# Performance work log

Hardware: AMD Instinct MI355X
Metric: run time of the kernel (lower is better)

Reference implementation:

```python
import jax, jax.numpy as jnp
import numpy as np

N = 256  # node_num, fully-connected graph
NEG_SLOPE = 0.2


def _edges(n):
    # fully-connected permutations; PyG GATConv removes then re-adds self-loops,
    # so effectively all n*n (src, dst) pairs are present.
    idx = jnp.arange(n)
    src = jnp.repeat(idx, n)
    dst = jnp.tile(idx, n)
    return src, dst


def _gat_conv(x, W, att_src, att_dst, b, src, dst, n):
    # x: [N, Fin], W: [Fin, H*C], att_*: [H, C], b: [H*C]
    H, C = att_src.shape
    h = (x @ W).reshape(n, H, C)                       # [N, H, C]
    a_src = jnp.einsum('nhc,hc->nh', h, att_src)       # [N, H]
    a_dst = jnp.einsum('nhc,hc->nh', h, att_dst)
    e = jax.nn.leaky_relu(a_src[src] + a_dst[dst], NEG_SLOPE)  # [E, H]
    # segment softmax over incoming edges of each dst node
    m = jax.ops.segment_max(e, dst, num_segments=n)    # [N, H]
    p = jnp.exp(e - m[dst])
    denom = jax.ops.segment_sum(p, dst, num_segments=n)
    alpha = p / (denom[dst] + 1e-16)                   # [E, H]
    msg = h[src] * alpha[:, :, None]                   # [E, H, C]
    out = jax.ops.segment_sum(msg, dst, num_segments=n)  # [N, H, C]
    return out.reshape(n, H * C) + b


def setup_inputs() -> dict:
    key = jax.random.key(0)
    ks = jax.random.split(key, 7)
    Fin, H1, C1 = 128, 4, 128
    s = lambda fan: 1.0 / np.sqrt(fan)
    return {
        'x': jax.random.normal(ks[0], (8, N, Fin), dtype=jnp.float32),
        'W1': jax.random.normal(ks[1], (Fin, H1 * C1), dtype=jnp.float32) * s(Fin),
        'att_src1': jax.random.normal(ks[2], (H1, C1), dtype=jnp.float32) * s(C1),
        'att_dst1': jax.random.normal(ks[3], (H1, C1), dtype=jnp.float32) * s(C1),
        'b1': jnp.zeros((H1 * C1,), dtype=jnp.float32),
        'W2': jax.random.normal(ks[4], (H1 * C1, Fin), dtype=jnp.float32) * s(H1 * C1),
        'att_src2': jax.random.normal(ks[5], (1, Fin), dtype=jnp.float32) * s(Fin),
        'att_dst2': jax.random.normal(ks[6], (1, Fin), dtype=jnp.float32) * s(Fin),
        'b2': jnp.zeros((Fin,), dtype=jnp.float32),
    }


def reference(x, W1, att_src1, att_dst1, b1, W2, att_src2, att_dst2, b2):
    src, dst = _edges(N)

    def one_graph(xi):
        h = jax.nn.relu(_gat_conv(xi, W1, att_src1, att_dst1, b1, src, dst, N))
        return _gat_conv(h, W2, att_src2, att_dst2, b2, src, dst, N)

    return jax.vmap(one_graph)(x)  # [B, N, Fin]
```

## Files before the change

kernel.cpp:

```cpp
#include <hip/hip_runtime.h>
#include <hip/hip_bf16.h>

#define BATCH 8
#define NN    256
#define FIN   128
#define H1    4
#define C1    128
#define HC1   512
#define NEG_SLOPE 0.2f

__global__ void gemm1_kernel(const float* __restrict__ x,
                             const float* __restrict__ W1,
                             float* __restrict__ h1) {
    __shared__ float xs[8][FIN];
    const int b  = blockIdx.y;
    const int r0 = blockIdx.x * 8;
    const int t  = threadIdx.x;

    const float* xp = x + (b * NN + r0) * FIN;
    #pragma unroll
    for (int i = 0; i < 4; ++i) {
        int idx = t + i * 256;
        xs[idx >> 7][idx & 127] = xp[idx];
    }
    __syncthreads();

    float acc[8][2];
    #pragma unroll
    for (int r = 0; r < 8; ++r) { acc[r][0] = 0.f; acc[r][1] = 0.f; }

    for (int k = 0; k < FIN; ++k) {
        float w0 = W1[k * HC1 + t];
        float w1 = W1[k * HC1 + t + 256];
        #pragma unroll
        for (int r = 0; r < 8; ++r) {
            float xv = xs[r][k];
            acc[r][0] = fmaf(xv, w0, acc[r][0]);
            acc[r][1] = fmaf(xv, w1, acc[r][1]);
        }
    }
    #pragma unroll
    for (int r = 0; r < 8; ++r) {
        h1[(b * NN + r0 + r) * HC1 + t]       = acc[r][0];
        h1[(b * NN + r0 + r) * HC1 + t + 256] = acc[r][1];
    }
}

__global__ void areduce1_kernel(const float* __restrict__ h1,
                                const float* __restrict__ att_src,
                                const float* __restrict__ att_dst,
                                float* __restrict__ a_src,
                                float* __restrict__ a_dst) {
    const int bn   = blockIdx.x;
    const int t    = threadIdx.x;
    const int h    = t >> 6;
    const int lane = t & 63;

    const float* hp = h1 + bn * HC1 + h * C1;
    float v0 = hp[lane], v1 = hp[lane + 64];
    float s = v0 * att_src[h * C1 + lane] + v1 * att_src[h * C1 + lane + 64];
    float d = v0 * att_dst[h * C1 + lane] + v1 * att_dst[h * C1 + lane + 64];
    #pragma unroll
    for (int off = 32; off > 0; off >>= 1) {
        s += __shfl_down(s, off, 64);
        d += __shfl_down(d, off, 64);
    }
    if (lane == 0) {
        a_src[bn * H1 + h] = s;
        a_dst[bn * H1 + h] = d;
    }
}

__global__ void agg1_kernel(const float* __restrict__ h1,
                            const float* __restrict__ a_src,
                            const float* __restrict__ a_dst,
                            const float* __restrict__ b1,
                            float* __restrict__ hrelu) {
    __shared__ float s_as[NN];
    __shared__ float s_ad[16];
    __shared__ float sp[16][NN];
    __shared__ float red[16][17];
    __shared__ float s_m[16], s_den[16];

    const int b    = blockIdx.z;
    const int head = blockIdx.y;
    const int d0   = blockIdx.x * 16;
    const int t    = threadIdx.x;

    s_as[t] = a_src[(b * NN + t) * H1 + head];
    if (t < 16) s_ad[t] = a_dst[(b * NN + d0 + t) * H1 + head];
    __syncthreads();

    const int d = t >> 4;
    const int l = t & 15;
    const float adst = s_ad[d];

    float mx = -1e30f;
    #pragma unroll
    for (int i = 0; i < 16; ++i) {
        int src = l + i * 16;
        float e = s_as[src] + adst;
        e = (e > 0.f) ? e : NEG_SLOPE * e;
        sp[d][src] = e;
        mx = fmaxf(mx, e);
    }
    red[d][l] = mx;
    __syncthreads();
    if (t < 16) {
        float m = red[t][0];
        #pragma unroll
        for (int i = 1; i < 16; ++i) m = fmaxf(m, red[t][i]);
        s_m[t] = m;
    }
    __syncthreads();

    const float m = s_m[d];
    float sum = 0.f;
    #pragma unroll
    for (int i = 0; i < 16; ++i) {
        int src = l + i * 16;
        float p = __expf(sp[d][src] - m);
        sp[d][src] = p;
        sum += p;
    }
    red[d][l] = sum;
    __syncthreads();
    if (t < 16) {
        float s = 0.f;
        #pragma unroll
        for (int i = 0; i < 16; ++i) s += red[t][i];
        s_den[t] = s + 1e-16f;
    }
    __syncthreads();

    const int c = t & 127;
    const int g = t >> 7;
    float acc[8];
    #pragma unroll
    for (int j = 0; j < 8; ++j) acc[j] = 0.f;

    const float* hbase = h1 + (size_t)(b * NN) * HC1 + head * C1 + c;
    for (int src = 0; src < NN; ++src) {
        float hv = hbase[(size_t)src * HC1];
        #pragma unroll
        for (int j = 0; j < 8; ++j)
            acc[j] = fmaf(sp[g * 8 + j][src], hv, acc[j]);
    }

    const float bias = b1[head * C1 + c];
    #pragma unroll
    for (int j = 0; j < 8; ++j) {
        int dst = d0 + g * 8 + j;
        float v = acc[j] / s_den[g * 8 + j] + bias;
        hrelu[(b * NN + dst) * HC1 + head * C1 + c] = fmaxf(v, 0.f);
    }
}

__global__ void gemm2_kernel(const float* __restrict__ hrelu,
                             const float* __restrict__ W2,
                             float* __restrict__ h2) {
    __shared__ float xs[8][HC1];
    const int b  = blockIdx.y;
    const int r0 = blockIdx.x * 8;
    const int t  = threadIdx.x;

    const float* xp = hrelu + (size_t)(b * NN + r0) * HC1;
    #pragma unroll
    for (int i = 0; i < 16; ++i) {
        int idx = t + i * 256;
        xs[idx >> 9][idx & 511] = xp[idx];
    }
    __syncthreads();

    const int c  = t & 127;
    const int rg = t >> 7;
    float acc[4];
    #pragma unroll
    for (int i = 0; i < 4; ++i) acc[i] = 0.f;

    for (int k = 0; k < HC1; ++k) {
        float w = W2[k * FIN + c];
        #pragma unroll
        for (int i = 0; i < 4; ++i)
            acc[i] = fmaf(xs[rg * 4 + i][k], w, acc[i]);
    }
    #pragma unroll
    for (int i = 0; i < 4; ++i)
        h2[(b * NN + r0 + rg * 4 + i) * FIN + c] = acc[i];
}

__global__ void areduce2_kernel(const float* __restrict__ h2,
                                const float* __restrict__ att_src,
                                const float* __restrict__ att_dst,
                                float* __restrict__ a_src,
                                float* __restrict__ a_dst) {
    const int t    = threadIdx.x;
    const int bn   = blockIdx.x * 4 + (t >> 6);
    const int lane = t & 63;

    const float* hp = h2 + bn * FIN;
    float v0 = hp[lane], v1 = hp[lane + 64];
    float s = v0 * att_src[lane] + v1 * att_src[lane + 64];
    float d = v0 * att_dst[lane] + v1 * att_dst[lane + 64];
    #pragma unroll
    for (int off = 32; off > 0; off >>= 1) {
        s += __shfl_down(s, off, 64);
        d += __shfl_down(d, off, 64);
    }
    if (lane == 0) {
        a_src[bn] = s;
        a_dst[bn] = d;
    }
}

__global__ void agg2_kernel(const float* __restrict__ h2,
                            const float* __restrict__ a_src,
                            const float* __restrict__ a_dst,
                            const float* __restrict__ b2,
                            float* __restrict__ out) {
    __shared__ float s_as[NN];
    __shared__ float s_ad[8];
    __shared__ float sp[8][NN];
    __shared__ float red[8][33];
    __shared__ float s_m[8], s_den[8];

    const int b  = blockIdx.y;
    const int d0 = blockIdx.x * 8;
    const int t  = threadIdx.x;

    s_as[t] = a_src[b * NN + t];
    if (t < 8) s_ad[t] = a_dst[b * NN + d0 + t];
    __syncthreads();

    const int d = t >> 5;
    const int l = t & 31;
    const float adst = s_ad[d];

    float mx = -1e30f;
    #pragma unroll
    for (int i = 0; i < 8; ++i) {
        int src = l + i * 32;
        float e = s_as[src] + adst;
        e = (e > 0.f) ? e : NEG_SLOPE * e;
        sp[d][src] = e;
        mx = fmaxf(mx, e);
    }
    red[d][l] = mx;
    __syncthreads();
    if (t < 8) {
        float m = red[t][0];
        #pragma unroll
        for (int i = 1; i < 32; ++i) m = fmaxf(m, red[t][i]);
        s_m[t] = m;
    }
    __syncthreads();

    const float m = s_m[d];
    float sum = 0.f;
    #pragma unroll
    for (int i = 0; i < 8; ++i) {
        int src = l + i * 32;
        float p = __expf(sp[d][src] - m);
        sp[d][src] = p;
        sum += p;
    }
    red[d][l] = sum;
    __syncthreads();
    if (t < 8) {
        float s = 0.f;
        #pragma unroll
        for (int i = 0; i < 32; ++i) s += red[t][i];
        s_den[t] = s + 1e-16f;
    }
    __syncthreads();

    const int c = t & 127;
    const int g = t >> 7;
    float acc[4];
    #pragma unroll
    for (int j = 0; j < 4; ++j) acc[j] = 0.f;

    const float* hbase = h2 + (size_t)(b * NN) * FIN + c;
    for (int src = 0; src < NN; ++src) {
        float hv = hbase[(size_t)src * FIN];
        #pragma unroll
        for (int j = 0; j < 4; ++j)
            acc[j] = fmaf(sp[g * 4 + j][src], hv, acc[j]);
    }

    const float bias = b2[c];
    #pragma unroll
    for (int j = 0; j < 4; ++j) {
        int dst = d0 + g * 4 + j;
        out[(b * NN + dst) * FIN + c] = acc[j] / s_den[g * 4 + j] + bias;
    }
}

extern "C" void kernel_launch(void* const* d_in, const int* in_sizes, int n_in,
                              void* d_out, int out_size, void* d_ws, size_t ws_size,
                              hipStream_t stream) {
    const float* x    = (const float*)d_in[0];
    const float* W1   = (const float*)d_in[1];
    const float* as1  = (const float*)d_in[2];
    const float* ad1  = (const float*)d_in[3];
    const float* b1   = (const float*)d_in[4];
    const float* W2   = (const float*)d_in[5];
    const float* as2  = (const float*)d_in[6];
    const float* ad2  = (const float*)d_in[7];
    const float* b2   = (const float*)d_in[8];
    float* out = (float*)d_out;

    float* ws = (float*)d_ws;
    float* h1     = ws;
    float* hrelu  = ws + 1048576;
    float* h2     = ws + 2097152;
    float* a_src1 = ws + 2359296;
    float* a_dst1 = ws + 2367488;
    float* a_src2 = ws + 2375680;
    float* a_dst2 = ws + 2377728;

    gemm1_kernel<<<dim3(32, BATCH), 256, 0, stream>>>(x, W1, h1);
    areduce1_kernel<<<BATCH * NN, 256, 0, stream>>>(h1, as1, ad1, a_src1, a_dst1);
    agg1_kernel<<<dim3(16, H1, BATCH), 256, 0, stream>>>(h1, a_src1, a_dst1, b1, hrelu);
    gemm2_kernel<<<dim3(32, BATCH), 256, 0, stream>>>(hrelu, W2, h2);
    areduce2_kernel<<<BATCH * NN / 4, 256, 0, stream>>>(h2, as2, ad2, a_src2, a_dst2);
    agg2_kernel<<<dim3(32, BATCH), 256, 0, stream>>>(h2, a_src2, a_dst2, b2, out);
}
```

Before: 141.4 us.

## Fuse attention-score reductions into GEMMs and retile aggregation kernels

Folds the per-node attention dot products (a_src/a_dst) into the epilogues of both GEMM kernels, which removes two separate launches and the re-read of h1/h2. All kernels move to 512-thread blocks with fewer rows per block, giving more blocks and more parallelism. The softmax reductions now use wave shuffles instead of shared-memory serial reductions, which cuts barriers. The trade-off is less register reuse per thread: each W or h load now feeds fewer accumulators, so memory traffic per FMA goes up.

```diff
diff --git a/kernel.cpp b/kernel.cpp
--- a/kernel.cpp
+++ b/kernel.cpp
@@ -9,305 +9,212 @@
 #define HC1   512
 #define NEG_SLOPE 0.2f
 
-__global__ void gemm1_kernel(const float* __restrict__ x,
-                             const float* __restrict__ W1,
-                             float* __restrict__ h1) {
-    __shared__ float xs[8][FIN];
-    const int b  = blockIdx.y;
-    const int r0 = blockIdx.x * 8;
-    const int t  = threadIdx.x;
-
-    const float* xp = x + (b * NN + r0) * FIN;
-    #pragma unroll
-    for (int i = 0; i < 4; ++i) {
-        int idx = t + i * 256;
-        xs[idx >> 7][idx & 127] = xp[idx];
-    }
-    __syncthreads();
-
-    float acc[8][2];
-    #pragma unroll
-    for (int r = 0; r < 8; ++r) { acc[r][0] = 0.f; acc[r][1] = 0.f; }
-
+__device__ __forceinline__ float lrelu(float v) {
+    return v > 0.f ? v : NEG_SLOPE * v;
+}
+
+__global__ __launch_bounds__(512, 4)
+void gemm1_fused(const float* __restrict__ x, const float* __restrict__ W1,
+                 const float* __restrict__ as1, const float* __restrict__ ad1,
+                 float* __restrict__ h1, float* __restrict__ a_src,
+                 float* __restrict__ a_dst) {
+    __shared__ float xs[4][FIN];
+    __shared__ float redS[4][8], redD[4][8];
+    const int b = blockIdx.y, r0 = blockIdx.x * 4, t = threadIdx.x;
+
+    xs[t >> 7][t & 127] = x[(b * NN + r0) * FIN + t];
+    __syncthreads();
+
+    float a0 = 0.f, a1 = 0.f, a2 = 0.f, a3 = 0.f;
+    #pragma unroll 8
     for (int k = 0; k < FIN; ++k) {
-        float w0 = W1[k * HC1 + t];
-        float w1 = W1[k * HC1 + t + 256];
+        float w = W1[k * HC1 + t];
+        a0 = fmaf(xs[0][k], w, a0);
+        a1 = fmaf(xs[1][k], w, a1);
+        a2 = fmaf(xs[2][k], w, a2);
+        a3 = fmaf(xs[3][k], w, a3);
+    }
+    float acc[4] = {a0, a1, a2, a3};
+    #pragma unroll
+    for (int r = 0; r < 4; ++r)
+        h1[(b * NN + r0 + r) * HC1 + t] = acc[r];
+
+    const float as = as1[t], ad = ad1[t];
+    const int w = t >> 6, lane = t & 63;
+    #pragma unroll
+    for (int r = 0; r < 4; ++r) {
+        float s = acc[r] * as, d = acc[r] * ad;
         #pragma unroll
-        for (int r = 0; r < 8; ++r) {
-            float xv = xs[r][k];
-            acc[r][0] = fmaf(xv, w0, acc[r][0]);
-            acc[r][1] = fmaf(xv, w1, acc[r][1]);
+        for (int off = 32; off > 0; off >>= 1) {
+            s += __shfl_down(s, off, 64);
+            d += __shfl_down(d, off, 64);
         }
-    }
-    #pragma unroll
-    for (int r = 0; r < 8; ++r) {
-        h1[(b * NN + r0 + r) * HC1 + t]       = acc[r][0];
-        h1[(b * NN + r0 + r) * HC1 + t + 256] = acc[r][1];
-    }
-}
-
-__global__ void areduce1_kernel(const float* __restrict__ h1,
-                                const float* __restrict__ att_src,
-                                const float* __restrict__ att_dst,
-                                float* __restrict__ a_src,
-                                float* __restrict__ a_dst) {
-    const int bn   = blockIdx.x;
-    const int t    = threadIdx.x;
-    const int h    = t >> 6;
-    const int lane = t & 63;
-
-    const float* hp = h1 + bn * HC1 + h * C1;
-    float v0 = hp[lane], v1 = hp[lane + 64];
-    float s = v0 * att_src[h * C1 + lane] + v1 * att_src[h * C1 + lane + 64];
-    float d = v0 * att_dst[h * C1 + lane] + v1 * att_dst[h * C1 + lane + 64];
+        if (lane == 0) { redS[r][w] = s; redD[r][w] = d; }
+    }
+    __syncthreads();
+    if (t < 16) {
+        int r = t & 3, h = t >> 2;
+        a_src[(b * NN + r0 + r) * H1 + h] = redS[r][2 * h] + redS[r][2 * h + 1];
+        a_dst[(b * NN + r0 + r) * H1 + h] = redD[r][2 * h] + redD[r][2 * h + 1];
+    }
+}
+
+__global__ __launch_bounds__(512, 4)
+void agg1_kernel(const float* __restrict__ h1, const float* __restrict__ a_src,
+                 const float* __restrict__ a_dst, const float* __restrict__ b1,
+                 float* __restrict__ hrelu) {
+    __shared__ float s_as[NN];
+    __shared__ float s_ad[16];
+    __shared__ float sp[16][NN];
+    __shared__ float s_den[16];
+
+    const int b = blockIdx.z, head = blockIdx.y, d0 = blockIdx.x * 16;
+    const int t = threadIdx.x;
+
+    if (t < NN) s_as[t] = a_src[(b * NN + t) * H1 + head];
+    if (t < 16) s_ad[t] = a_dst[(b * NN + d0 + t) * H1 + head];
+    __syncthreads();
+
+    const int d = t >> 5, l = t & 31;
+    const float adst = s_ad[d];
+    float e[8];
+    float mx = -1e30f;
+    #pragma unroll
+    for (int i = 0; i < 8; ++i) {
+        float v = lrelu(s_as[l + i * 32] + adst);
+        e[i] = v;
+        mx = fmaxf(mx, v);
+    }
+    #pragma unroll
+    for (int off = 16; off > 0; off >>= 1)
+        mx = fmaxf(mx, __shfl_down(mx, off, 32));
+    mx = __shfl(mx, 0, 32);
+    float sum = 0.f;
+    #pragma unroll
+    for (int i = 0; i < 8; ++i) {
+        float p = __expf(e[i] - mx);
+        sp[d][l + i * 32] = p;
+        sum += p;
+    }
+    #pragma unroll
+    for (int off = 16; off > 0; off >>= 1)
+        sum += __shfl_down(sum, off, 32);
+    if (l == 0) s_den[d] = sum + 1e-16f;
+    __syncthreads();
+
+    const int c = t & 127, g = t >> 7;
+    float c0 = 0.f, c1 = 0.f, c2 = 0.f, c3 = 0.f;
+    const float* hb = h1 + (size_t)(b * NN) * HC1 + head * C1 + c;
+    #pragma unroll 4
+    for (int src = 0; src < NN; ++src) {
+        float hv = hb[(size_t)src * HC1];
+        c0 = fmaf(sp[g * 4 + 0][src], hv, c0);
+        c1 = fmaf(sp[g * 4 + 1][src], hv, c1);
+        c2 = fmaf(sp[g * 4 + 2][src], hv, c2);
+        c3 = fmaf(sp[g * 4 + 3][src], hv, c3);
+    }
+    float accs[4] = {c0, c1, c2, c3};
+    const float bias = b1[head * C1 + c];
+    #pragma unroll
+    for (int j = 0; j < 4; ++j) {
+        int dst = d0 + g * 4 + j;
+        float v = accs[j] / s_den[g * 4 + j] + bias;
+        hrelu[(b * NN + dst) * HC1 + head * C1 + c] = fmaxf(v, 0.f);
+    }
+}
+
+__global__ __launch_bounds__(512, 4)
+void gemm2_fused(const float* __restrict__ hrelu, const float* __restrict__ W2,
+                 const float* __restrict__ as2, const float* __restrict__ ad2,
+                 float* __restrict__ h2, float* __restrict__ a_src,
+                 float* __restrict__ a_dst) {
+    __shared__ float xs[4][HC1];
+    __shared__ float redS[4][2], redD[4][2];
+    const int b = blockIdx.y, r0 = blockIdx.x * 4, t = threadIdx.x;
+
+    const float4* xp = (const float4*)(hrelu + (size_t)(b * NN + r0) * HC1);
+    ((float4*)xs)[t] = xp[t];
+    __syncthreads();
+
+    const int c = t & 127, rg = t >> 7;
+    float acc = 0.f;
+    #pragma unroll 8
+    for (int k = 0; k < HC1; ++k)
+        acc = fmaf(xs[rg][k], W2[k * FIN + c], acc);
+    h2[(b * NN + r0 + rg) * FIN + c] = acc;
+
+    float s = acc * as2[c], d = acc * ad2[c];
+    const int lane = t & 63, w = (t >> 6) & 1;
     #pragma unroll
     for (int off = 32; off > 0; off >>= 1) {
         s += __shfl_down(s, off, 64);
         d += __shfl_down(d, off, 64);
     }
-    if (lane == 0) {
-        a_src[bn * H1 + h] = s;
-        a_dst[bn * H1 + h] = d;
-    }
-}
-
-__global__ void agg1_kernel(const float* __restrict__ h1,
-                            const float* __restrict__ a_src,
-                            const float* __restrict__ a_dst,
-                            const float* __restrict__ b1,
-                            float* __restrict__ hrelu) {
+    if (lane == 0) { redS[rg][w] = s; redD[rg][w] = d; }
+    __syncthreads();
+    if (t < 4) {
+        a_src[b * NN + r0 + t] = redS[t][0] + redS[t][1];
+        a_dst[b * NN + r0 + t] = redD[t][0] + redD[t][1];
+    }
+}
+
+__global__ __launch_bounds__(512, 4)
+void agg2_kernel(const float* __restrict__ h2, const float* __restrict__ a_src,
+                 const float* __restrict__ a_dst, const float* __restrict__ b2,
+                 float* __restrict__ out) {
     __shared__ float s_as[NN];
-    __shared__ float s_ad[16];
-    __shared__ float sp[16][NN];
-    __shared__ float red[16][17];
-    __shared__ float s_m[16], s_den[16];
-
-    const int b    = blockIdx.z;
-    const int head = blockIdx.y;
-    const int d0   = blockIdx.x * 16;
-    const int t    = threadIdx.x;
-
-    s_as[t] = a_src[(b * NN + t) * H1 + head];
-    if (t < 16) s_ad[t] = a_dst[(b * NN + d0 + t) * H1 + head];
-    __syncthreads();
-
-    const int d = t >> 4;
-    const int l = t & 15;
+    __shared__ float s_ad[4];
+    __shared__ float sp[4][NN];
+    __shared__ float redm[4][2], reds[4][2];
+
+    const int b = blockIdx.y, d0 = blockIdx.x * 4, t = threadIdx.x;
+
+    if (t < NN) s_as[t] = a_src[b * NN + t];
+    if (t < 4) s_ad[t] = a_dst[b * NN + d0 + t];
+    __syncthreads();
+
+    const int d = t >> 7, l = t & 127, lane = t & 63, w = (t >> 6) & 1;
     const float adst = s_ad[d];
-
-    float mx = -1e30f;
-    #pragma unroll
-    for (int i = 0; i < 16; ++i) {
-        int src = l + i * 16;
-        float e = s_as[src] + adst;
-        e = (e > 0.f) ? e : NEG_SLOPE * e;
-        sp[d][src] = e;
-        mx = fmaxf(mx, e);
-    }
-    red[d][l] = mx;
-    __syncthreads();
-    if (t < 16) {
-        float m = red[t][0];
-        #pragma unroll
-        for (int i = 1; i < 16; ++i) m = fmaxf(m, red[t][i]);
-        s_m[t] = m;
-    }
-    __syncthreads();
-
-    const float m = s_m[d];
-    float sum = 0.f;
-    #pragma unroll
-    for (int i = 0; i < 16; ++i) {
-        int src = l + i * 16;
-        float p = __expf(sp[d][src] - m);
-        sp[d][src] = p;
-        sum += p;
-    }
-    red[d][l] = sum;
-    __syncthreads();
-    if (t < 16) {
-        float s = 0.f;
-        #pragma unroll
-        for (int i = 0; i < 16; ++i) s += red[t][i];
-        s_den[t] = s + 1e-16f;
-    }
-    __syncthreads();
-
-    const int c = t & 127;
-    const int g = t >> 7;
-    float acc[8];
-    #pragma unroll
-    for (int j = 0; j < 8; ++j) acc[j] = 0.f;
-
-    const float* hbase = h1 + (size_t)(b * NN) * HC1 + head * C1 + c;
-    for (int src = 0; src < NN; ++src) {
-        float hv = hbase[(size_t)src * HC1];
-        #pragma unroll
-        for (int j = 0; j < 8; ++j)
-            acc[j] = fmaf(sp[g * 8 + j][src], hv, acc[j]);
-    }
-
-    const float bias = b1[head * C1 + c];
-    #pragma unroll
-    for (int j = 0; j < 8; ++j) {
-        int dst = d0 + g * 8 + j;
-        float v = acc[j] / s_den[g * 8 + j] + bias;
-        hrelu[(b * NN + dst) * HC1 + head * C1 + c] = fmaxf(v, 0.f);
-    }
-}
-
-__global__ void gemm2_kernel(const float* __restrict__ hrelu,
-                             const float* __restrict__ W2,
-                             float* __restrict__ h2) {
-    __shared__ float xs[8][HC1];
-    const int b  = blockIdx.y;
-    const int r0 = blockIdx.x * 8;
-    const int t  = threadIdx.x;
-
-    const float* xp = hrelu + (size_t)(b * NN + r0) * HC1;
-    #pragma unroll
-    for (int i = 0; i < 16; ++i) {
-        int idx = t + i * 256;
-        xs[idx >> 9][idx & 511] = xp[idx];
-    }
-    __syncthreads();
-
-    const int c  = t & 127;
-    const int rg = t >> 7;
-    float acc[4];
-    #pragma unroll
-    for (int i = 0; i < 4; ++i) acc[i] = 0.f;
-
-    for (int k = 0; k < HC1; ++k) {
-        float w = W2[k * FIN + c];
-        #pragma unroll
-        for (int i = 0; i < 4; ++i)
-            acc[i] = fmaf(xs[rg * 4 + i][k], w, acc[i]);
-    }
-    #pragma unroll
-    for (int i = 0; i < 4; ++i)
-        h2[(b * NN + r0 + rg * 4 + i) * FIN + c] = acc[i];
-}
-
-__global__ void areduce2_kernel(const float* __restrict__ h2,
-                                const float* __restrict__ att_src,
-                                const float* __restrict__ att_dst,
-                                float* __restrict__ a_src,
-                                float* __restrict__ a_dst) {
-    const int t    = threadIdx.x;
-    const int bn   = blockIdx.x * 4 + (t >> 6);
-    const int lane = t & 63;
-
-    const float* hp = h2 + bn * FIN;
-    float v0 = hp[lane], v1 = hp[lane + 64];
-    float s = v0 * att_src[lane] + v1 * att_src[lane + 64];
-    float d = v0 * att_dst[lane] + v1 * att_dst[lane + 64];
-    #pragma unroll
-    for (int off = 32; off > 0; off >>= 1) {
-        s += __shfl_down(s, off, 64);
-        d += __shfl_down(d, off, 64);
-    }
-    if (lane == 0) {
-        a_src[bn] = s;
-        a_dst[bn] = d;
-    }
-}
-
-__global__ void agg2_kernel(const float* __restrict__ h2,
-                            const float* __restrict__ a_src,
-                            const float* __restrict__ a_dst,
-                            const float* __restrict__ b2,
-                            float* __restrict__ out) {
-    __shared__ float s_as[NN];
-    __shared__ float s_ad[8];
-    __shared__ float sp[8][NN];
-    __shared__ float red[8][33];
-    __shared__ float s_m[8], s_den[8];
-
-    const int b  = blockIdx.y;
-    const int d0 = blockIdx.x * 8;
-    const int t  = threadIdx.x;
-
-    s_as[t] = a_src[b * NN + t];
-    if (t < 8) s_ad[t] = a_dst[b * NN + d0 + t];
-    __syncthreads();
-
-    const int d = t >> 5;
-    const int l = t & 31;
-    const float adst = s_ad[d];
-
-    float mx = -1e30f;
-    #pragma unroll
-    for (int i = 0; i < 8; ++i) {
-        int src = l + i * 32;
-        float e = s_as[src] + adst;
-        e = (e > 0.f) ? e : NEG_SLOPE * e;
-        sp[d][src] = e;
-        mx = fmaxf(mx, e);
-    }
-    red[d][l] = mx;
-    __syncthreads();
-    if (t < 8) {
-        float m = red[t][0];
-        #pragma unroll
-        for (int i = 1; i < 32; ++i) m = fmaxf(m, red[t][i]);
-        s_m[t] = m;
-    }
-    __syncthreads();
-
-    const float m = s_m[d];
-    float sum = 0.f;
-    #pragma unroll
-    for (int i = 0; i < 8; ++i) {
-        int src = l + i * 32;
-        float p = __expf(sp[d][src] - m);
-        sp[d][src] = p;
-        sum += p;
-    }
-    red[d][l] = sum;
-    __syncthreads();
-    if (t < 8) {
-        float s = 0.f;
-        #pragma unroll
-        for (int i = 0; i < 32; ++i) s += red[t][i];
-        s_den[t] = s + 1e-16f;
-    }
-    __syncthreads();
-
-    const int c = t & 127;
-    const int g = t >> 7;
-    float acc[4];
-    #pragma unroll
-    for (int j = 0; j < 4; ++j) acc[j] = 0.f;
-
-    const float* hbase = h2 + (size_t)(b * NN) * FIN + c;
-    for (int src = 0; src < NN; ++src) {
-        float hv = hbase[(size_t)src * FIN];
-        #pragma unroll
-        for (int j = 0; j < 4; ++j)
-            acc[j] = fmaf(sp[g * 4 + j][src], hv, acc[j]);
-    }
-
-    const float bias = b2[c];
-    #pragma unroll
-    for (int j = 0; j < 4; ++j) {
-        int dst = d0 + g * 4 + j;
-        out[(b * NN + dst) * FIN + c] = acc[j] / s_den[g * 4 + j] + bias;
-    }
+    float e0 = lrelu(s_as[l] + adst);
+    float e1 = lrelu(s_as[l + 128] + adst);
+    float mx = fmaxf(e0, e1);
+    #pragma unroll
+    for (int off = 32; off > 0; off >>= 1)
+        mx = fmaxf(mx, __shfl_down(mx, off, 64));
+    if (lane == 0) redm[d][w] = mx;
+    __syncthreads();
+    const float m = fmaxf(redm[d][0], redm[d][1]);
+    float p0 = __expf(e0 - m), p1 = __expf(e1 - m);
+    sp[d][l] = p0;
+    sp[d][l + 128] = p1;
+    float sum = p0 + p1;
+    #pragma unroll
+    for (int off = 32; off > 0; off >>= 1)
+        sum += __shfl_down(sum, off, 64);
+    if (lane == 0) reds[d][w] = sum;
+    __syncthreads();
+    const float den = reds[d][0] + reds[d][1] + 1e-16f;
+
+    float acc = 0.f;
+    const float* hb = h2 + (size_t)(b * NN) * FIN + l;
+    #pragma unroll 4
+    for (int src = 0; src < NN; ++src)
+        acc = fmaf(sp[d][src], hb[(size_t)src * FIN], acc);
+    out[(b * NN + d0 + d) * FIN + l] = acc / den + b2[l];
 }
 
 extern "C" void kernel_launch(void* const* d_in, const int* in_sizes, int n_in,
                               void* d_out, int out_size, void* d_ws, size_t ws_size,
                               hipStream_t stream) {
-    const float* x    = (const float*)d_in[0];
-    const float* W1   = (const float*)d_in[1];
-    const float* as1  = (const float*)d_in[2];
-    const float* ad1  = (const float*)d_in[3];
-    const float* b1   = (const float*)d_in[4];
-    const float* W2   = (const float*)d_in[5];
-    const float* as2  = (const float*)d_in[6];
-    const float* ad2  = (const float*)d_in[7];
-    const float* b2   = (const float*)d_in[8];
+    const float* x   = (const float*)d_in[0];
+    const float* W1  = (const float*)d_in[1];
+    const float* as1 = (const float*)d_in[2];
+    const float* ad1 = (const float*)d_in[3];
+    const float* b1  = (const float*)d_in[4];
+    const float* W2  = (const float*)d_in[5];
+    const float* as2 = (const float*)d_in[6];
+    const float* ad2 = (const float*)d_in[7];
+    const float* b2  = (const float*)d_in[8];
     float* out = (float*)d_out;
 
     float* ws = (float*)d_ws;
@@ -319,10 +226,8 @@
     float* a_src2 = ws + 2375680;
     float* a_dst2 = ws + 2377728;
 
-    gemm1_kernel<<<dim3(32, BATCH), 256, 0, stream>>>(x, W1, h1);
-    areduce1_kernel<<<BATCH * NN, 256, 0, stream>>>(h1, as1, ad1, a_src1, a_dst1);
-    agg1_kernel<<<dim3(16, H1, BATCH), 256, 0, stream>>>(h1, a_src1, a_dst1, b1, hrelu);
-    gemm2_kernel<<<dim3(32, BATCH), 256, 0, stream>>>(hrelu, W2, h2);
-    areduce2_kernel<<<BATCH * NN / 4, 256, 0, stream>>>(h2, as2, ad2, a_src2, a_dst2);
-    agg2_kernel<<<dim3(32, BATCH), 256, 0, stream>>>(h2, a_src2, a_dst2, b2, out);
-}
+    gemm1_fused<<<dim3(64, BATCH), 512, 0, stream>>>(x, W1, as1, ad1, h1, a_src1, a_dst1);
+    agg1_kernel<<<dim3(16, H1, BATCH), 512, 0, stream>>>(h1, a_src1, a_dst1, b1, hrelu);
+    gemm2_fused<<<dim3(64, BATCH), 512, 0, stream>>>(hrelu, W2, as2, ad2, h2, a_src2, a_dst2);
+    agg2_kernel<<<dim3(64, BATCH), 512, 0, stream>>>(h2, a_src2, a_dst2, b2, out);
+}
```

After: 146.5 us. 1.04x slower.
